# Kernel tuning notes

Hardware: AMD Instinct MI355X
Metric: run time of the kernel (lower is better)

## Reference

```python
import jax, jax.numpy as jnp
import numpy as np

EMBED_DIM = 1024
NUM_HEADS = 16
D_K = EMBED_DIM // NUM_HEADS
SEQ = 4096
BATCH = 1


def setup_inputs() -> dict:
    key = jax.random.key(0)
    ks = jax.random.split(key, 9)
    s = 1.0 / np.sqrt(EMBED_DIM)
    return {
        "x": jax.random.normal(ks[0], (BATCH, SEQ, EMBED_DIM), dtype=jnp.float32),
        "Wq": jax.random.normal(ks[1], (EMBED_DIM, EMBED_DIM), dtype=jnp.float32) * s,
        "bq": jax.random.normal(ks[2], (EMBED_DIM,), dtype=jnp.float32) * 0.02,
        "Wk": jax.random.normal(ks[3], (EMBED_DIM, EMBED_DIM), dtype=jnp.float32) * s,
        "bk": jax.random.normal(ks[4], (EMBED_DIM,), dtype=jnp.float32) * 0.02,
        "Wv": jax.random.normal(ks[5], (EMBED_DIM, EMBED_DIM), dtype=jnp.float32) * s,
        "bv": jax.random.normal(ks[6], (EMBED_DIM,), dtype=jnp.float32) * 0.02,
        "Wo": jax.random.normal(ks[7], (EMBED_DIM, EMBED_DIM), dtype=jnp.float32) * s,
        "bo": jax.random.normal(ks[8], (EMBED_DIM,), dtype=jnp.float32) * 0.02,
    }


def reference(x, Wq, bq, Wk, bk, Wv, bv, Wo, bo):
    B, S, E = x.shape
    H, Dk = NUM_HEADS, D_K

    def split_heads(t):  # [B,S,E] -> [B,H,S,Dk]
        return t.reshape(B, S, H, Dk).transpose(0, 2, 1, 3)

    Q = split_heads(x @ Wq.T + bq)
    K = split_heads(x @ Wk.T + bk)
    V = split_heads(x @ Wv.T + bv)

    scores = jnp.einsum("bhqd,bhkd->bhqk", Q, K) / jnp.sqrt(jnp.float32(Dk))
    causal = jnp.tril(jnp.ones((S, S), dtype=bool))
    scores = jnp.where(causal, scores, -jnp.inf)
    attn = jax.nn.softmax(scores, axis=-1)
    out = jnp.einsum("bhqk,bhkd->bhqd", attn, V)  # [B,H,S,Dk]
    out = out.transpose(0, 2, 1, 3).reshape(B, S, E)
    return out @ Wo.T + bo
```

## Files before the change

kernel.cpp:

```cpp
#include <hip/hip_runtime.h>
#include <hip/hip_bf16.h>
#include <math.h>

#define SEQ 4096
#define EMB 1024
#define NH  16
#define DK  64

typedef __attribute__((ext_vector_type(8))) unsigned short us8;
typedef __attribute__((ext_vector_type(8))) short         s8;
typedef __attribute__((ext_vector_type(4))) unsigned short us4;
typedef __attribute__((ext_vector_type(4))) float          f4;

static __device__ __forceinline__ unsigned short f2bf(float f) {
    union { float f; unsigned u; } v; v.f = f;
    unsigned r = v.u + 0x7FFF + ((v.u >> 16) & 1);
    return (unsigned short)(r >> 16);
}

__device__ __forceinline__ void gl2lds16(const void* g, void* l) {
    __builtin_amdgcn_global_load_lds((const __attribute__((address_space(1))) void*)g,
                                     (__attribute__((address_space(3))) void*)l, 16, 0, 0);
}

__device__ __forceinline__ int pkbf(float a, float b) {
    return (int)__builtin_amdgcn_perm(__float_as_uint(a), __float_as_uint(b), 0x07060302u);
}

__global__ void cvt_all(const float* __restrict__ x,
                        const float* __restrict__ w0, const float* __restrict__ w1,
                        const float* __restrict__ w2, const float* __restrict__ w3,
                        unsigned short* __restrict__ xo,
                        unsigned short* __restrict__ o0, unsigned short* __restrict__ o1,
                        unsigned short* __restrict__ o2, unsigned short* __restrict__ o3) {
    const int idx = blockIdx.x * 256 + threadIdx.x;
    const float* in;
    unsigned short* out;
    int off;
    if (idx < (1 << 20)) { in = x; out = xo; off = idx; }
    else {
        const int t = idx - (1 << 20);
        const int w = t >> 18;
        off = t & ((1 << 18) - 1);
        in  = w == 0 ? w0 : (w == 1 ? w1 : (w == 2 ? w2 : w3));
        out = w == 0 ? o0 : (w == 1 ? o1 : (w == 2 ? o2 : o3));
    }
    const float4 v = ((const float4*)in)[off];
    us4 o;
    o[0] = f2bf(v.x); o[1] = f2bf(v.y); o[2] = f2bf(v.z); o[3] = f2bf(v.w);
    ((us4*)out)[off] = o;
}

__global__ __launch_bounds__(256) void qkv_gemm(
    const unsigned short* __restrict__ X,
    const unsigned short* __restrict__ Wq, const unsigned short* __restrict__ Wk,
    const unsigned short* __restrict__ Wv,
    const float* __restrict__ bq, const float* __restrict__ bk, const float* __restrict__ bv,
    unsigned short* __restrict__ Qo, unsigned short* __restrict__ Ko, unsigned short* __restrict__ Vto)
{
    __shared__ unsigned short As[128 * 64];
    __shared__ unsigned short Bs[128 * 64];

    const int flat = blockIdx.y * 32 + blockIdx.x;
    const int wg   = (flat & 7) * 96 + (flat >> 3);
    const int bxi  = wg & 31;
    const int byi  = wg >> 5;

    const int region = byi >> 3;
    const unsigned short* W   = region == 0 ? Wq : (region == 1 ? Wk : Wv);
    const float*         bias = region == 0 ? bq : (region == 1 ? bk : bv);
    const float scale = region == 0 ? 0.18033688011112042f : 1.0f;

    const int tid  = threadIdx.x;
    const int wave = tid >> 6;
    const int lane = tid & 63;
    const int quad = lane >> 4;
    const int l16  = lane & 15;
    const int wm   = (wave >> 1) * 64;
    const int wn   = (wave & 1) * 64;
    const int bm   = bxi * 128;
    const int bn   = (byi & 7) * 128;

    f4 acc[4][4];
#pragma unroll
    for (int a = 0; a < 4; ++a)
#pragma unroll
        for (int b = 0; b < 4; ++b) acc[a][b] = (f4){0, 0, 0, 0};

    const int rsub = lane >> 3;
    const int gc   = ((lane & 7) ^ rsub) * 8;
    const int swz  = l16 & 7;

    for (int k0 = 0; k0 < EMB; k0 += 64) {
        __syncthreads();
#pragma unroll
        for (int i = 0; i < 4; ++i) {
            const int cb = i * 4 + wave;
            const int r  = cb * 8 + rsub;
            gl2lds16(X + (size_t)(bm + r) * EMB + k0 + gc, &As[cb * 512]);
            gl2lds16(W + (size_t)(bn + r) * EMB + k0 + gc, &Bs[cb * 512]);
        }
        __syncthreads();
        if (region != 2) {
#pragma unroll
            for (int kc = 0; kc < 2; ++kc) {
                s8 af[4], bf[4];
#pragma unroll
                for (int t = 0; t < 4; ++t) {
                    const int seg = (kc * 4 + quad) ^ swz;
                    af[t] = *(const s8*)&As[(wm + t * 16 + l16) * 64 + seg * 8];
                    bf[t] = *(const s8*)&Bs[(wn + t * 16 + l16) * 64 + seg * 8];
                }
#pragma unroll
                for (int tm = 0; tm < 4; ++tm)
#pragma unroll
                    for (int tn = 0; tn < 4; ++tn)
                        acc[tm][tn] = __builtin_amdgcn_mfma_f32_16x16x32_bf16(bf[tn], af[tm], acc[tm][tn], 0, 0, 0);
            }
        } else {
#pragma unroll
            for (int kc = 0; kc < 2; ++kc) {
                s8 af[4], bf[4];
#pragma unroll
                for (int t = 0; t < 4; ++t) {
                    const int seg = (kc * 4 + quad) ^ swz;
                    af[t] = *(const s8*)&As[(wm + t * 16 + l16) * 64 + seg * 8];
                    bf[t] = *(const s8*)&Bs[(wn + t * 16 + l16) * 64 + seg * 8];
                }
#pragma unroll
                for (int tm = 0; tm < 4; ++tm)
#pragma unroll
                    for (int tn = 0; tn < 4; ++tn)
                        acc[tm][tn] = __builtin_amdgcn_mfma_f32_16x16x32_bf16(af[tm], bf[tn], acc[tm][tn], 0, 0, 0);
            }
        }
    }

    if (region == 2) {
#pragma unroll
        for (int tn = 0; tn < 4; ++tn) {
            const int n = bn + wn + tn * 16 + l16;
            const float bv2 = bias[n];
            unsigned short* dst = Vto + (size_t)n * SEQ + bm + (wm & 64) + quad * 8;
            us8 ov;
#pragma unroll
            for (int rr = 0; rr < 4; ++rr) {
                ov[rr]     = f2bf(acc[0][tn][rr] + bv2);
                ov[4 + rr] = f2bf(acc[1][tn][rr] + bv2);
            }
            *(us8*)dst = ov;
#pragma unroll
            for (int rr = 0; rr < 4; ++rr) {
                ov[rr]     = f2bf(acc[2][tn][rr] + bv2);
                ov[4 + rr] = f2bf(acc[3][tn][rr] + bv2);
            }
            *(us8*)(dst + 32) = ov;
        }
    } else {
        unsigned short* out = region == 0 ? Qo : Ko;
#pragma unroll
        for (int tn = 0; tn < 4; ++tn) {
            const int n4 = bn + wn + tn * 16 + quad * 4;
            const f4 bv4 = *(const f4*)&bias[n4];
#pragma unroll
            for (int tm = 0; tm < 4; ++tm) {
                const int m = bm + wm + tm * 16 + l16;
                us4 ov;
#pragma unroll
                for (int rr = 0; rr < 4; ++rr) ov[rr] = f2bf((acc[tm][tn][rr] + bv4[rr]) * scale);
                *(us4*)&out[(size_t)m * EMB + n4] = ov;
            }
        }
    }
}

__global__ __launch_bounds__(256) void gemm_op(
    const unsigned short* __restrict__ A, const unsigned short* __restrict__ B,
    const float* __restrict__ bias, float* __restrict__ C)
{
    __shared__ unsigned short As[128 * 64];
    __shared__ unsigned short Bs[64 * 64];

    const int flat = blockIdx.y * 32 + blockIdx.x;
    const int wg   = (flat & 7) * 64 + (flat >> 3);
    const int bxi  = wg & 31;
    const int byi  = wg >> 5;

    const int tid  = threadIdx.x;
    const int wave = tid >> 6;
    const int lane = tid & 63;
    const int quad = lane >> 4;
    const int l16  = lane & 15;
    const int wm   = (wave >> 1) * 64;
    const int wn   = (wave & 1) * 32;
    const int bm   = bxi * 128;
    const int bn   = byi * 64;

    f4 acc[4][2];
#pragma unroll
    for (int a = 0; a < 4; ++a) { acc[a][0] = (f4){0,0,0,0}; acc[a][1] = (f4){0,0,0,0}; }

    const int rsub = lane >> 3;
    const int gc   = ((lane & 7) ^ rsub) * 8;
    const int swz  = l16 & 7;

    for (int k0 = 0; k0 < EMB; k0 += 64) {
        __syncthreads();
#pragma unroll
        for (int i = 0; i < 6; ++i) {
            const int cb = i * 4 + wave;
            if (cb < 16) {
                gl2lds16(A + (size_t)(bm + cb * 8 + rsub) * EMB + k0 + gc, &As[cb * 512]);
            } else {
                const int c2 = cb - 16;
                gl2lds16(B + (size_t)(bn + c2 * 8 + rsub) * EMB + k0 + gc, &Bs[c2 * 512]);
            }
        }
        __syncthreads();
#pragma unroll
        for (int kc = 0; kc < 2; ++kc) {
            const int seg = (kc * 4 + quad) ^ swz;
            s8 af[4], bf[2];
#pragma unroll
            for (int t = 0; t < 4; ++t)
                af[t] = *(const s8*)&As[(wm + t * 16 + l16) * 64 + seg * 8];
#pragma unroll
            for (int t = 0; t < 2; ++t)
                bf[t] = *(const s8*)&Bs[(wn + t * 16 + l16) * 64 + seg * 8];
#pragma unroll
            for (int tm = 0; tm < 4; ++tm)
#pragma unroll
                for (int tn = 0; tn < 2; ++tn)
                    acc[tm][tn] = __builtin_amdgcn_mfma_f32_16x16x32_bf16(bf[tn], af[tm], acc[tm][tn], 0, 0, 0);
        }
    }

#pragma unroll
    for (int tn = 0; tn < 2; ++tn) {
        const int n4 = bn + wn + tn * 16 + quad * 4;
        const f4 bv4 = *(const f4*)&bias[n4];
#pragma unroll
        for (int tm = 0; tm < 4; ++tm) {
            const int m = bm + wm + tm * 16 + l16;
            f4 v = acc[tm][tn] + bv4;
            *(f4*)&C[(size_t)m * EMB + n4] = v;
        }
    }
}

__global__ __launch_bounds__(512, 4) void attn_kernel(
    const unsigned short* __restrict__ Qg, const unsigned short* __restrict__ Kg,
    const unsigned short* __restrict__ Vtg, unsigned short* __restrict__ Og)
{
    __shared__ unsigned short Ks[2][2][64][64];
    __shared__ unsigned short Vs[2][2][64][64];

    const int tid  = threadIdx.x;
    const int wave = tid >> 6;
    const int lane = tid & 63;
    const int quad = lane >> 4;
    const int l16  = lane & 15;
    const int h    = blockIdx.x;
    const int y    = blockIdx.y;
    const int u    = (y < 16) ? y : 47 - y;
    const int jmax = 63 - u;
    const int tileMine = (wave < 4) ? (63 - u) : u;
    const int par  = (wave >> 1) & 1;
    const int qh   = wave & 1;
    const int jmine = tileMine;
    const int colbase = h * DK;
    const int wrow0 = tileMine * 64 + qh * 32;
    const int q0    = wrow0 + l16;

    s8 qf00, qf10, qf01, qf11;
    {
        const unsigned short* q = Qg + (size_t)q0 * EMB + colbase + quad * 8;
        qf00 = *(const s8*)(q);
        qf10 = *(const s8*)(q + 32);
        qf01 = *(const s8*)(q + (size_t)16 * EMB);
        qf11 = *(const s8*)(q + (size_t)16 * EMB + 32);
    }

    const int xr    = (l16 & 7) << 4;
    const int coff0 = ((quad * 16) ^ xr) >> 1;
    const int coff1 = (((64) + quad * 16) ^ xr) >> 1;

    const int srow = tid >> 3;
    const int scol = (((tid & 7) * 16) ^ ((srow & 7) << 4)) >> 1;
    const unsigned short* ksrc = Kg  + (size_t)srow * EMB + colbase + scol;
    const unsigned short* vsrc = Vtg + (size_t)(colbase + srow) * SEQ + scol;

    const int imax = jmax >> 1;

    gl2lds16(ksrc,                    &Ks[0][0][wave * 8][0]);
    gl2lds16(vsrc,                    &Vs[0][0][wave * 8][0]);
    gl2lds16(ksrc + (size_t)64 * EMB, &Ks[0][1][wave * 8][0]);
    gl2lds16(vsrc + 64,               &Vs[0][1][wave * 8][0]);

    float l0 = 0.0f, l1 = 0.0f;
    f4 o0[4], o1[4];
#pragma unroll
    for (int t = 0; t < 4; ++t) { o0[t] = (f4){0, 0, 0, 0}; o1[t] = (f4){0, 0, 0, 0}; }

    for (int i = 0; i <= imax; ++i) {
        __syncthreads();
        const int cur = i & 1;
        if (i < imax) {
            const int nxt = cur ^ 1;
            const int je  = 2 * (i + 1);
            gl2lds16(ksrc + (size_t)je * 64 * EMB, &Ks[nxt][0][wave * 8][0]);
            gl2lds16(vsrc + (size_t)je * 64,       &Vs[nxt][0][wave * 8][0]);
            const int jo = je + 1;
            if (jo <= jmax) {
                gl2lds16(ksrc + (size_t)jo * 64 * EMB, &Ks[nxt][1][wave * 8][0]);
                gl2lds16(vsrc + (size_t)jo * 64,       &Vs[nxt][1][wave * 8][0]);
            }
        }

        const int j = 2 * i + par;
        if (j <= jmine) {
            const unsigned short* KsP = &Ks[cur][par][0][0];
            const unsigned short* VsP = &Vs[cur][par][0][0];

            f4 s0[4] = { {0,0,0,0}, {0,0,0,0}, {0,0,0,0}, {0,0,0,0} };
            f4 s1[4] = { {0,0,0,0}, {0,0,0,0}, {0,0,0,0}, {0,0,0,0} };
            __builtin_amdgcn_s_setprio(1);
#pragma unroll
            for (int t = 0; t < 4; ++t) {
                const int rbase = (t * 16 + l16) * 64;
                s8 kv0 = *(const s8*)&KsP[rbase + coff0];
                s8 kv1 = *(const s8*)&KsP[rbase + coff1];
                s0[t] = __builtin_amdgcn_mfma_f32_16x16x32_bf16(kv0, qf00, s0[t], 0, 0, 0);
                s1[t] = __builtin_amdgcn_mfma_f32_16x16x32_bf16(kv0, qf01, s1[t], 0, 0, 0);
                s0[t] = __builtin_amdgcn_mfma_f32_16x16x32_bf16(kv1, qf10, s0[t], 0, 0, 0);
                s1[t] = __builtin_amdgcn_mfma_f32_16x16x32_bf16(kv1, qf11, s1[t], 0, 0, 0);
            }
            __builtin_amdgcn_s_setprio(0);

            if (j == jmine) {
#pragma unroll
                for (int t = 0; t < 4; ++t) {
                    const int kb = j * 64 + t * 16 + quad * 4;
#pragma unroll
                    for (int r = 0; r < 4; ++r) {
                        if (kb + r > q0)      s0[t][r] = -1e30f;
                        if (kb + r > q0 + 16) s1[t][r] = -1e30f;
                    }
                }
            }

            float rs0 = 0.0f, rs1 = 0.0f;
#pragma unroll
            for (int t = 0; t < 4; ++t)
#pragma unroll
                for (int r = 0; r < 4; ++r) {
                    const float p0 = __builtin_amdgcn_exp2f(s0[t][r]);
                    const float p1 = __builtin_amdgcn_exp2f(s1[t][r]);
                    s0[t][r] = p0; rs0 += p0;
                    s1[t][r] = p1; rs1 += p1;
                }
            rs0 += __shfl_xor(rs0, 16);
            rs0 += __shfl_xor(rs0, 32);
            rs1 += __shfl_xor(rs1, 16);
            rs1 += __shfl_xor(rs1, 32);
            l0 += rs0;
            l1 += rs1;

            union { int i[8]; s8 v[2]; } pk0, pk1;
#pragma unroll
            for (int t = 0; t < 4; ++t) {
                pk0.i[t * 2]     = pkbf(s0[t][1], s0[t][0]);
                pk0.i[t * 2 + 1] = pkbf(s0[t][3], s0[t][2]);
                pk1.i[t * 2]     = pkbf(s1[t][1], s1[t][0]);
                pk1.i[t * 2 + 1] = pkbf(s1[t][3], s1[t][2]);
            }

            __builtin_amdgcn_s_setprio(1);
#pragma unroll
            for (int t = 0; t < 4; ++t) {
                const int rbase = (t * 16 + l16) * 64;
                s8 va0 = *(const s8*)&VsP[rbase + coff0];
                s8 va1 = *(const s8*)&VsP[rbase + coff1];
                o0[t] = __builtin_amdgcn_mfma_f32_16x16x32_bf16(va0, pk0.v[0], o0[t], 0, 0, 0);
                o1[t] = __builtin_amdgcn_mfma_f32_16x16x32_bf16(va0, pk1.v[0], o1[t], 0, 0, 0);
                o0[t] = __builtin_amdgcn_mfma_f32_16x16x32_bf16(va1, pk0.v[1], o0[t], 0, 0, 0);
                o1[t] = __builtin_amdgcn_mfma_f32_16x16x32_bf16(va1, pk1.v[1], o1[t], 0, 0, 0);
            }
            __builtin_amdgcn_s_setprio(0);
        }
    }

    __syncthreads();
    float* mO = (float*)&Ks[0][0][0][0];
    float* mL = (float*)&Vs[0][0][0][0];
    const int slot = (wave >> 2) * 2 + qh;
    const int mrow = slot * 64 + lane;
    char* mp = (char*)mO + (size_t)mrow * 128;
    const int msw = (lane & 7) << 4;
    if (par == 1) {
#pragma unroll
        for (int t = 0; t < 4; ++t) {
            *(f4*)(mp + ((t * 32)      ^ msw)) = o0[t];
            *(f4*)(mp + ((t * 32 + 16) ^ msw)) = o1[t];
        }
        mL[mrow * 2]     = l0;
        mL[mrow * 2 + 1] = l1;
    }
    __syncthreads();
    if (par == 0) {
#pragma unroll
        for (int t = 0; t < 4; ++t) {
            o0[t] += *(const f4*)(mp + ((t * 32)      ^ msw));
            o1[t] += *(const f4*)(mp + ((t * 32 + 16) ^ msw));
        }
        l0 += mL[mrow * 2];
        l1 += mL[mrow * 2 + 1];
        const float inv0 = 1.0f / l0;
        const float inv1 = 1.0f / l1;
#pragma unroll
        for (int t = 0; t < 4; ++t) {
            us4 ov;
#pragma unroll
            for (int r = 0; r < 4; ++r) ov[r] = f2bf(o0[t][r] * inv0);
            *(us4*)&Og[(size_t)q0 * EMB + colbase + t * 16 + quad * 4] = ov;
#pragma unroll
            for (int r = 0; r < 4; ++r) ov[r] = f2bf(o1[t][r] * inv1);
            *(us4*)&Og[(size_t)(q0 + 16) * EMB + colbase + t * 16 + quad * 4] = ov;
        }
    }
}

extern "C" void kernel_launch(void* const* d_in, const int* in_sizes, int n_in,
                              void* d_out, int out_size, void* d_ws, size_t ws_size,
                              hipStream_t stream) {
    const float* x  = (const float*)d_in[0];
    const float* Wq = (const float*)d_in[1];
    const float* bq = (const float*)d_in[2];
    const float* Wk = (const float*)d_in[3];
    const float* bk = (const float*)d_in[4];
    const float* Wv = (const float*)d_in[5];
    const float* bv = (const float*)d_in[6];
    const float* Wo = (const float*)d_in[7];
    const float* bo = (const float*)d_in[8];
    float* out = (float*)d_out;

    unsigned short* ws = (unsigned short*)d_ws;
    unsigned short* xb  = ws;
    unsigned short* Wqb = xb  + (size_t)SEQ * EMB;
    unsigned short* Wkb = Wqb + (size_t)EMB * EMB;
    unsigned short* Wvb = Wkb + (size_t)EMB * EMB;
    unsigned short* Wob = Wvb + (size_t)EMB * EMB;
    unsigned short* Qb  = Wob + (size_t)EMB * EMB;
    unsigned short* Kb  = Qb  + (size_t)SEQ * EMB;
    unsigned short* Vtb = Kb  + (size_t)SEQ * EMB;
    unsigned short* Ab  = Vtb + (size_t)SEQ * EMB;

    cvt_all<<<8192, 256, 0, stream>>>(x, Wq, Wk, Wv, Wo, xb, Wqb, Wkb, Wvb, Wob);

    qkv_gemm<<<dim3(SEQ / 128, 24), 256, 0, stream>>>(xb, Wqb, Wkb, Wvb, bq, bk, bv, Qb, Kb, Vtb);

    attn_kernel<<<dim3(NH, 32), 512, 0, stream>>>(Qb, Kb, Vtb, Ab);

    gemm_op<<<dim3(SEQ / 128, EMB / 64), 256, 0, stream>>>(Ab, Wob, bo, out);
}
```

Baseline: 201.7 us.

## Give each attention wave 64 query rows with 4 waves per block

The attention block shrinks from 8 waves to 4, and each wave now owns a full 64-row query tile (4 query sub-tiles) instead of 32 rows. Every K/V fragment read from LDS is reused across four MFMA chains instead of two, which halves LDS read traffic per unit of work. Each wave also issues four staging loads per tile pair instead of two. The cost is many more accumulator and score registers per wave, and fewer waves per block to hide latency, which may lower occupancy.

```diff
diff --git a/kernel.cpp b/kernel.cpp
--- a/kernel.cpp
+++ b/kernel.cpp
@@ -248,7 +248,7 @@
     }
 }
 
-__global__ __launch_bounds__(512, 4) void attn_kernel(
+__global__ __launch_bounds__(256, 2) void attn_kernel(
     const unsigned short* __restrict__ Qg, const unsigned short* __restrict__ Kg,
     const unsigned short* __restrict__ Vtg, unsigned short* __restrict__ Og)
 {
@@ -264,43 +264,51 @@
     const int y    = blockIdx.y;
     const int u    = (y < 16) ? y : 47 - y;
     const int jmax = 63 - u;
-    const int tileMine = (wave < 4) ? (63 - u) : u;
-    const int par  = (wave >> 1) & 1;
-    const int qh   = wave & 1;
-    const int jmine = tileMine;
-    const int colbase = h * DK;
-    const int wrow0 = tileMine * 64 + qh * 32;
-    const int q0    = wrow0 + l16;
-
-    s8 qf00, qf10, qf01, qf11;
-    {
-        const unsigned short* q = Qg + (size_t)q0 * EMB + colbase + quad * 8;
-        qf00 = *(const s8*)(q);
-        qf10 = *(const s8*)(q + 32);
-        qf01 = *(const s8*)(q + (size_t)16 * EMB);
-        qf11 = *(const s8*)(q + (size_t)16 * EMB + 32);
+    const int par  = wave & 1;
+    const bool isA = wave < 2;
+    const int tileMine = isA ? jmax : u;
+    const int jmine    = tileMine;
+    const int colbase  = h * DK;
+    const int q0       = tileMine * 64 + l16;
+
+    s8 qf[4][2];
+#pragma unroll
+    for (int qn = 0; qn < 4; ++qn) {
+        const unsigned short* q = Qg + (size_t)(q0 + 16 * qn) * EMB + colbase + quad * 8;
+        qf[qn][0] = *(const s8*)(q);
+        qf[qn][1] = *(const s8*)(q + 32);
     }
 
     const int xr    = (l16 & 7) << 4;
     const int coff0 = ((quad * 16) ^ xr) >> 1;
-    const int coff1 = (((64) + quad * 16) ^ xr) >> 1;
+    const int coff1 = ((64 + quad * 16) ^ xr) >> 1;
 
     const int srow = tid >> 3;
     const int scol = (((tid & 7) * 16) ^ ((srow & 7) << 4)) >> 1;
     const unsigned short* ksrc = Kg  + (size_t)srow * EMB + colbase + scol;
     const unsigned short* vsrc = Vtg + (size_t)(colbase + srow) * SEQ + scol;
+    const int ldo = wave * 512;
+
+#define STAGE_PAIR(buf, sub, jt) do {                                              \
+        unsigned short* kD = &Ks[buf][sub][0][0];                                  \
+        unsigned short* vD = &Vs[buf][sub][0][0];                                  \
+        gl2lds16(ksrc + (size_t)(jt) * 64 * EMB,        kD + ldo);                 \
+        gl2lds16(ksrc + (size_t)((jt) * 64 + 32) * EMB, kD + 2048 + ldo);          \
+        gl2lds16(vsrc + (jt) * 64,                      vD + ldo);                 \
+        gl2lds16(vsrc + (size_t)32 * SEQ + (jt) * 64,   vD + 2048 + ldo);          \
+    } while (0)
 
     const int imax = jmax >> 1;
 
-    gl2lds16(ksrc,                    &Ks[0][0][wave * 8][0]);
-    gl2lds16(vsrc,                    &Vs[0][0][wave * 8][0]);
-    gl2lds16(ksrc + (size_t)64 * EMB, &Ks[0][1][wave * 8][0]);
-    gl2lds16(vsrc + 64,               &Vs[0][1][wave * 8][0]);
-
-    float l0 = 0.0f, l1 = 0.0f;
-    f4 o0[4], o1[4];
-#pragma unroll
-    for (int t = 0; t < 4; ++t) { o0[t] = (f4){0, 0, 0, 0}; o1[t] = (f4){0, 0, 0, 0}; }
+    STAGE_PAIR(0, 0, 0);
+    STAGE_PAIR(0, 1, 1);
+
+    float l[4] = {0.f, 0.f, 0.f, 0.f};
+    f4 o[4][4];
+#pragma unroll
+    for (int qn = 0; qn < 4; ++qn)
+#pragma unroll
+        for (int t = 0; t < 4; ++t) o[qn][t] = (f4){0, 0, 0, 0};
 
     for (int i = 0; i <= imax; ++i) {
         __syncthreads();
@@ -308,13 +316,9 @@
         if (i < imax) {
             const int nxt = cur ^ 1;
             const int je  = 2 * (i + 1);
-            gl2lds16(ksrc + (size_t)je * 64 * EMB, &Ks[nxt][0][wave * 8][0]);
-            gl2lds16(vsrc + (size_t)je * 64,       &Vs[nxt][0][wave * 8][0]);
+            STAGE_PAIR(nxt, 0, je);
             const int jo = je + 1;
-            if (jo <= jmax) {
-                gl2lds16(ksrc + (size_t)jo * 64 * EMB, &Ks[nxt][1][wave * 8][0]);
-                gl2lds16(vsrc + (size_t)jo * 64,       &Vs[nxt][1][wave * 8][0]);
-            }
+            if (jo <= jmax) STAGE_PAIR(nxt, 1, jo);
         }
 
         const int j = 2 * i + par;
@@ -322,18 +326,23 @@
             const unsigned short* KsP = &Ks[cur][par][0][0];
             const unsigned short* VsP = &Vs[cur][par][0][0];
 
-            f4 s0[4] = { {0,0,0,0}, {0,0,0,0}, {0,0,0,0}, {0,0,0,0} };
-            f4 s1[4] = { {0,0,0,0}, {0,0,0,0}, {0,0,0,0}, {0,0,0,0} };
+            f4 s[4][4];
+#pragma unroll
+            for (int qn = 0; qn < 4; ++qn)
+#pragma unroll
+                for (int t = 0; t < 4; ++t) s[qn][t] = (f4){0, 0, 0, 0};
+
             __builtin_amdgcn_s_setprio(1);
 #pragma unroll
             for (int t = 0; t < 4; ++t) {
                 const int rbase = (t * 16 + l16) * 64;
                 s8 kv0 = *(const s8*)&KsP[rbase + coff0];
                 s8 kv1 = *(const s8*)&KsP[rbase + coff1];
-                s0[t] = __builtin_amdgcn_mfma_f32_16x16x32_bf16(kv0, qf00, s0[t], 0, 0, 0);
-                s1[t] = __builtin_amdgcn_mfma_f32_16x16x32_bf16(kv0, qf01, s1[t], 0, 0, 0);
-                s0[t] = __builtin_amdgcn_mfma_f32_16x16x32_bf16(kv1, qf10, s0[t], 0, 0, 0);
-                s1[t] = __builtin_amdgcn_mfma_f32_16x16x32_bf16(kv1, qf11, s1[t], 0, 0, 0);
+#pragma unroll
+                for (int qn = 0; qn < 4; ++qn) {
+                    s[qn][t] = __builtin_amdgcn_mfma_f32_16x16x32_bf16(kv0, qf[qn][0], s[qn][t], 0, 0, 0);
+                    s[qn][t] = __builtin_amdgcn_mfma_f32_16x16x32_bf16(kv1, qf[qn][1], s[qn][t], 0, 0, 0);
+                }
             }
             __builtin_amdgcn_s_setprio(0);
 
@@ -342,38 +351,39 @@
                 for (int t = 0; t < 4; ++t) {
                     const int kb = j * 64 + t * 16 + quad * 4;
 #pragma unroll
+                    for (int r = 0; r < 4; ++r)
+#pragma unroll
+                        for (int qn = 0; qn < 4; ++qn)
+                            if (kb + r > q0 + 16 * qn) s[qn][t][r] = -1e30f;
+                }
+            }
+
+            float rs[4] = {0.f, 0.f, 0.f, 0.f};
+#pragma unroll
+            for (int qn = 0; qn < 4; ++qn)
+#pragma unroll
+                for (int t = 0; t < 4; ++t)
+#pragma unroll
                     for (int r = 0; r < 4; ++r) {
-                        if (kb + r > q0)      s0[t][r] = -1e30f;
-                        if (kb + r > q0 + 16) s1[t][r] = -1e30f;
+                        const float p = __builtin_amdgcn_exp2f(s[qn][t][r]);
+                        s[qn][t][r] = p;
+                        rs[qn] += p;
                     }
-                }
-            }
-
-            float rs0 = 0.0f, rs1 = 0.0f;
-#pragma unroll
-            for (int t = 0; t < 4; ++t)
-#pragma unroll
-                for (int r = 0; r < 4; ++r) {
-                    const float p0 = __builtin_amdgcn_exp2f(s0[t][r]);
-                    const float p1 = __builtin_amdgcn_exp2f(s1[t][r]);
-                    s0[t][r] = p0; rs0 += p0;
-                    s1[t][r] = p1; rs1 += p1;
-                }
-            rs0 += __shfl_xor(rs0, 16);
-            rs0 += __shfl_xor(rs0, 32);
-            rs1 += __shfl_xor(rs1, 16);
-            rs1 += __shfl_xor(rs1, 32);
-            l0 += rs0;
-            l1 += rs1;
-
-            union { int i[8]; s8 v[2]; } pk0, pk1;
-#pragma unroll
-            for (int t = 0; t < 4; ++t) {
-                pk0.i[t * 2]     = pkbf(s0[t][1], s0[t][0]);
-                pk0.i[t * 2 + 1] = pkbf(s0[t][3], s0[t][2]);
-                pk1.i[t * 2]     = pkbf(s1[t][1], s1[t][0]);
-                pk1.i[t * 2 + 1] = pkbf(s1[t][3], s1[t][2]);
-            }
+#pragma unroll
+            for (int qn = 0; qn < 4; ++qn) {
+                rs[qn] += __shfl_xor(rs[qn], 16);
+                rs[qn] += __shfl_xor(rs[qn], 32);
+                l[qn] += rs[qn];
+            }
+
+            union { int i[8]; s8 v[2]; } pk[4];
+#pragma unroll
+            for (int qn = 0; qn < 4; ++qn)
+#pragma unroll
+                for (int t = 0; t < 4; ++t) {
+                    pk[qn].i[t * 2]     = pkbf(s[qn][t][1], s[qn][t][0]);
+                    pk[qn].i[t * 2 + 1] = pkbf(s[qn][t][3], s[qn][t][2]);
+                }
 
             __builtin_amdgcn_s_setprio(1);
 #pragma unroll
@@ -381,51 +391,47 @@
                 const int rbase = (t * 16 + l16) * 64;
                 s8 va0 = *(const s8*)&VsP[rbase + coff0];
                 s8 va1 = *(const s8*)&VsP[rbase + coff1];
-                o0[t] = __builtin_amdgcn_mfma_f32_16x16x32_bf16(va0, pk0.v[0], o0[t], 0, 0, 0);
-                o1[t] = __builtin_amdgcn_mfma_f32_16x16x32_bf16(va0, pk1.v[0], o1[t], 0, 0, 0);
-                o0[t] = __builtin_amdgcn_mfma_f32_16x16x32_bf16(va1, pk0.v[1], o0[t], 0, 0, 0);
-                o1[t] = __builtin_amdgcn_mfma_f32_16x16x32_bf16(va1, pk1.v[1], o1[t], 0, 0, 0);
+#pragma unroll
+                for (int qn = 0; qn < 4; ++qn) {
+                    o[qn][t] = __builtin_amdgcn_mfma_f32_16x16x32_bf16(va0, pk[qn].v[0], o[qn][t], 0, 0, 0);
+                    o[qn][t] = __builtin_amdgcn_mfma_f32_16x16x32_bf16(va1, pk[qn].v[1], o[qn][t], 0, 0, 0);
+                }
             }
             __builtin_amdgcn_s_setprio(0);
         }
     }
+#undef STAGE_PAIR
 
     __syncthreads();
     float* mO = (float*)&Ks[0][0][0][0];
     float* mL = (float*)&Vs[0][0][0][0];
-    const int slot = (wave >> 2) * 2 + qh;
+    const int slot = isA ? 0 : 1;
     const int mrow = slot * 64 + lane;
-    char* mp = (char*)mO + (size_t)mrow * 128;
+    char* mp = (char*)mO + (size_t)mrow * 256;
     const int msw = (lane & 7) << 4;
     if (par == 1) {
 #pragma unroll
-        for (int t = 0; t < 4; ++t) {
-            *(f4*)(mp + ((t * 32)      ^ msw)) = o0[t];
-            *(f4*)(mp + ((t * 32 + 16) ^ msw)) = o1[t];
-        }
-        mL[mrow * 2]     = l0;
-        mL[mrow * 2 + 1] = l1;
+        for (int qn = 0; qn < 4; ++qn) {
+#pragma unroll
+            for (int t = 0; t < 4; ++t)
+                *(f4*)(mp + ((qn * 64 + t * 16) ^ msw)) = o[qn][t];
+            mL[mrow * 4 + qn] = l[qn];
+        }
     }
     __syncthreads();
     if (par == 0) {
 #pragma unroll
-        for (int t = 0; t < 4; ++t) {
-            o0[t] += *(const f4*)(mp + ((t * 32)      ^ msw));
-            o1[t] += *(const f4*)(mp + ((t * 32 + 16) ^ msw));
-        }
-        l0 += mL[mrow * 2];
-        l1 += mL[mrow * 2 + 1];
-        const float inv0 = 1.0f / l0;
-        const float inv1 = 1.0f / l1;
-#pragma unroll
-        for (int t = 0; t < 4; ++t) {
-            us4 ov;
-#pragma unroll
-            for (int r = 0; r < 4; ++r) ov[r] = f2bf(o0[t][r] * inv0);
-            *(us4*)&Og[(size_t)q0 * EMB + colbase + t * 16 + quad * 4] = ov;
-#pragma unroll
-            for (int r = 0; r < 4; ++r) ov[r] = f2bf(o1[t][r] * inv1);
-            *(us4*)&Og[(size_t)(q0 + 16) * EMB + colbase + t * 16 + quad * 4] = ov;
+        for (int qn = 0; qn < 4; ++qn) {
+            const float lq  = l[qn] + mL[mrow * 4 + qn];
+            const float inv = 1.0f / lq;
+#pragma unroll
+            for (int t = 0; t < 4; ++t) {
+                f4 v = o[qn][t] + *(const f4*)(mp + ((qn * 64 + t * 16) ^ msw));
+                us4 ov;
+#pragma unroll
+                for (int r = 0; r < 4; ++r) ov[r] = f2bf(v[r] * inv);
+                *(us4*)&Og[(size_t)(q0 + 16 * qn) * EMB + colbase + t * 16 + quad * 4] = ov;
+            }
         }
     }
 }
@@ -459,7 +465,7 @@
 
     qkv_gemm<<<dim3(SEQ / 128, 24), 256, 0, stream>>>(xb, Wqb, Wkb, Wvb, bq, bk, bv, Qb, Kb, Vtb);
 
-    attn_kernel<<<dim3(NH, 32), 512, 0, stream>>>(Qb, Kb, Vtb, Ab);
+    attn_kernel<<<dim3(NH, 32), 256, 0, stream>>>(Qb, Kb, Vtb, Ab);
 
     gemm_op<<<dim3(SEQ / 128, EMB / 64), 256, 0, stream>>>(Ab, Wob, bo, out);
 }
```

Result: slower. 217.5 us (+7.8%).
